# Performance work log

Measured on AMD Instinct MI355X. Metric: run time of the kernel, lower is better.

Reference implementation:

```python
import jax, jax.numpy as jnp
import numpy as np

# dims
N, T = 16, 2000            # batch, encoder frames
ENC, DEC = 512, 512        # enc_dim, dec_dim
ATT, C, K, H = 512, 10, 64, 4  # att_dim, conv_channels, loc_context, att_head


def setup_inputs() -> dict:
    key = jax.random.key(0)
    ks = jax.random.split(key, 16)
    s = 0.02
    enc_pad = jax.random.normal(ks[0], (N, T, ENC), jnp.float32)
    enc_len = jax.random.randint(ks[1], (N,), T // 2, T + 1, jnp.int32)
    dec_prev = jax.random.normal(ks[2], (N, DEC), jnp.float32)
    ali_prev = jax.random.uniform(ks[3], (N, H, T), jnp.float32)
    ali_prev = ali_prev / ali_prev.sum(-1, keepdims=True)
    # parameters (torch layout)
    We = jax.random.normal(ks[4], (ATT * H, ENC), jnp.float32) * s   # enc_proj weight
    be = jnp.zeros((ATT * H,), jnp.float32)                          # enc_proj bias
    Wk = jax.random.normal(ks[5], (ATT * H, ENC), jnp.float32) * s   # key_proj
    Wd = jax.random.normal(ks[6], (ATT * H, DEC), jnp.float32) * s   # dec_proj
    WF = jax.random.normal(ks[7], (C * H, 1, 2 * K + 1), jnp.float32) * s  # F: grouped conv1d
    bF = jnp.zeros((C * H,), jnp.float32)
    Wa = jax.random.normal(ks[8], (H, ATT, C), jnp.float32) * s      # att: 1x1 grouped conv, per-head [ATT,C]
    Ww = jax.random.normal(ks[9], (H, ATT), jnp.float32) * s         # w: 1x1 grouped conv, per-head [ATT]
    Wc = jax.random.normal(ks[10], (ENC, ATT * H), jnp.float32) * s  # ctx_proj
    bc = jnp.zeros((ENC,), jnp.float32)
    return {"enc_pad": enc_pad, "enc_len": enc_len, "dec_prev": dec_prev,
            "ali_prev": ali_prev, "We": We, "be": be, "Wk": Wk, "Wd": Wd,
            "WF": WF, "bF": bF, "Wa": Wa, "Ww": Ww, "Wc": Wc, "bc": bc}


def reference(enc_pad, enc_len, dec_prev, ali_prev, We, be, Wk, Wd, WF, bF, Wa, Ww, Wc, bc):
    n, t, _ = enc_pad.shape
    # enc_part: N x H x T x D
    ep = enc_pad @ We.T + be
    enc_part = ep.reshape(n, t, H, ATT).transpose(0, 2, 1, 3)
    # key_part: N x H x D x T (matches torch transpose(1,2).view ordering)
    kp = enc_pad @ Wk.T
    key_part = kp.transpose(0, 2, 1).reshape(n, H, ATT, t)
    # pad mask: N x T, True where padded
    pad_mask = jnp.arange(t)[None, :] >= enc_len[:, None]
    # location features: grouped conv1d over alignment, per head
    f = jax.lax.conv_general_dilated(
        ali_prev, WF, window_strides=(1,), padding=[(K, K)],
        dimension_numbers=("NCH", "OIH", "NCH"), feature_group_count=H)
    f = (f + bF[None, :, None]).reshape(n, H, C, t)
    # 1x1 grouped conv: C -> ATT per head
    att_part = jnp.einsum("hdc,nhct->nhdt", Wa, f)
    dec_part = (dec_prev @ Wd.T).reshape(n, H, ATT)
    sum_part = jnp.tanh(att_part + key_part + dec_part[..., None])  # N x H x D x T
    score = jnp.einsum("hd,nhdt->nht", Ww, sum_part)                # N x H x T
    score = jnp.where(pad_mask[:, None, :], -jnp.inf, score)
    ali = jax.nn.softmax(score, axis=-1)
    ctx = jnp.einsum("nht,nhtd->nhd", ali, enc_part).reshape(n, H * ATT)
    ctx = ctx @ Wc.T + bc
    return ali, ctx
```

## Files before the change

### kernel.cpp

```cpp
#include <hip/hip_runtime.h>

#define NB   16
#define TT   2000
#define TP   2048
#define SPT  2048
#define ENC  512
#define ATTD 512
#define HH   4
#define CC   10
#define KK   64
#define KW   129
#define HATT 2048

typedef unsigned short u16;
typedef __attribute__((ext_vector_type(8))) short bf16x8;
typedef __attribute__((ext_vector_type(4))) float f32x4;

#define AS1 __attribute__((address_space(1)))
#define AS3 __attribute__((address_space(3)))

__device__ inline unsigned bfpack2(float lo, float hi) {
    unsigned a = __builtin_bit_cast(unsigned, lo);
    unsigned b = __builtin_bit_cast(unsigned, hi);
    a = (a + 0x7fffu + ((a >> 16) & 1u)) >> 16;
    b = (b + 0x7fffu + ((b >> 16) & 1u)) >> 16;
    return a | (b << 16);
}

__global__ __launch_bounds__(256) void prep_kernel(
    const float* __restrict__ enc, const float* __restrict__ Wk,
    const float* __restrict__ ali_prev, const float* __restrict__ WF,
    const float* __restrict__ bF, const float* __restrict__ dec_prev,
    const float* __restrict__ Wd, const float* __restrict__ Wa,
    const int* __restrict__ enc_len,
    u16* __restrict__ Abf, u16* __restrict__ Wkbf,
    u16* __restrict__ ftb, u16* __restrict__ wab,
    float* __restrict__ decp)
{
    __shared__ union {
        struct { float aliW[632]; float wfT[KW * CC]; float bfs[CC]; } cv;
        float dsl[16 * 128];
    } sm;
    const int bid = blockIdx.x, tid = threadIdx.x;

    if (bid < 8704) {
        long long gid = ((long long)bid * 256 + tid) * 8;
        const long long ATOT = (long long)NB * TP * ENC;
        if (gid < ATOT) {
            int n = (int)(gid >> 20);
            int rem = (int)(gid & ((1 << 20) - 1));
            int r = rem >> 9, e = rem & 511;
            if (r < enc_len[n]) {
                const float* s = enc + ((long long)n * TT + r) * ENC + e;
                float4 v0 = *(const float4*)s;
                float4 v1 = *(const float4*)(s + 4);
                uint4 out;
                out.x = bfpack2(v0.x, v0.y); out.y = bfpack2(v0.z, v0.w);
                out.z = bfpack2(v1.x, v1.y); out.w = bfpack2(v1.z, v1.w);
                *(uint4*)(Abf + gid) = out;
            }
        } else {
            long long j = gid - ATOT;
            const float* s = Wk + j;
            float4 v0 = *(const float4*)s;
            float4 v1 = *(const float4*)(s + 4);
            uint4 out;
            out.x = bfpack2(v0.x, v0.y); out.y = bfpack2(v0.z, v0.w);
            out.z = bfpack2(v1.x, v1.y); out.w = bfpack2(v1.z, v1.w);
            *(uint4*)(Wkbf + j) = out;
        }
    } else if (bid < 8960) {
        int b2 = bid - 8704;
        int tc = b2 & 3, h = (b2 >> 2) & 3, n = b2 >> 4;
        int t0 = tc * 500;
        float* aliW = sm.cv.aliW;
        float* wfT  = sm.cv.wfT;
        float* bfs  = sm.cv.bfs;
        const float* arow = ali_prev + ((long long)n * HH + h) * TT;
        for (int i = tid; i < 632; i += 256) {
            int tt = t0 - KK + i;
            aliW[i] = (tt >= 0 && tt < TT) ? arow[tt] : 0.f;
        }
        for (int i = tid; i < KW * CC; i += 256) {
            int k = i / CC, c = i - k * CC;
            wfT[i] = WF[(h * CC + c) * KW + k];
        }
        if (tid < CC) bfs[tid] = bF[h * CC + tid];
        __syncthreads();
        if (tid < 250) {
            float acc0[CC], acc1[CC];
            #pragma unroll
            for (int c = 0; c < CC; c++) { acc0[c] = 0.f; acc1[c] = 0.f; }
            const int base = 2 * tid;
            float2 w0 = *(const float2*)&aliW[base];
            for (int k = 0; k < 128; k += 2) {
                float2 w2 = *(const float2*)&aliW[base + k + 2];
                #pragma unroll
                for (int cj = 0; cj < 5; cj++) {
                    float2 fk  = *(const float2*)&wfT[k * CC + cj * 2];
                    float2 fk1 = *(const float2*)&wfT[(k + 1) * CC + cj * 2];
                    acc0[2*cj]   += w0.x * fk.x + w0.y * fk1.x;
                    acc0[2*cj+1] += w0.x * fk.y + w0.y * fk1.y;
                    acc1[2*cj]   += w0.y * fk.x + w2.x * fk1.x;
                    acc1[2*cj+1] += w0.y * fk.y + w2.x * fk1.y;
                }
                w0 = w2;
            }
            #pragma unroll
            for (int cj = 0; cj < 5; cj++) {
                float2 fk = *(const float2*)&wfT[128 * CC + cj * 2];
                acc0[2*cj]   += w0.x * fk.x;  acc0[2*cj+1] += w0.x * fk.y;
                acc1[2*cj]   += w0.y * fk.x;  acc1[2*cj+1] += w0.y * fk.y;
            }
            #pragma unroll
            for (int c = 0; c < CC; c++) { acc0[c] += bfs[c]; acc1[c] += bfs[c]; }
            int t = t0 + base;
            u16* frow = ftb + (((long long)(n * HH + h)) * TP + t) * 16;
            uint4 ra, rb;
            ra.x = bfpack2(acc0[0], acc0[1]); ra.y = bfpack2(acc0[2], acc0[3]);
            ra.z = bfpack2(acc0[4], acc0[5]); ra.w = bfpack2(acc0[6], acc0[7]);
            rb.x = bfpack2(acc0[8], acc0[9]); rb.y = 0u; rb.z = 0u; rb.w = 0u;
            *(uint4*)(frow)     = ra; *(uint4*)(frow + 8)  = rb;
            ra.x = bfpack2(acc1[0], acc1[1]); ra.y = bfpack2(acc1[2], acc1[3]);
            ra.z = bfpack2(acc1[4], acc1[5]); ra.w = bfpack2(acc1[6], acc1[7]);
            rb.x = bfpack2(acc1[8], acc1[9]);
            *(uint4*)(frow + 16) = ra; *(uint4*)(frow + 24) = rb;
        } else if (tc == 3) {
            uint4 z = {0u, 0u, 0u, 0u};
            int r0 = 2000 + (tid - 250) * 8;
            u16* frow = ftb + (((long long)(n * HH + h)) * TP + r0) * 16;
            for (int r = 0; r < 8; r++) {
                *(uint4*)(frow + r * 16)     = z;
                *(uint4*)(frow + r * 16 + 8) = z;
            }
        }
    } else if (bid < 8992) {
        int b2 = bid - 8960;
        int kc = b2 >> 3, jc = b2 & 7;
        for (int i = tid; i < 2048; i += 256) {
            int nn = i >> 7, kk = i & 127;
            sm.dsl[i] = dec_prev[nn * 512 + kc * 128 + kk];
        }
        __syncthreads();
        int d = jc * 256 + tid;
        float acc[NB];
        #pragma unroll
        for (int n = 0; n < NB; n++) acc[n] = 0.f;
        const float4* w4 = (const float4*)(Wd + (long long)d * 512 + kc * 128);
        for (int e4 = 0; e4 < 32; e4++) {
            float4 w = w4[e4];
            #pragma unroll
            for (int n = 0; n < NB; n++) {
                const float* a = sm.dsl + n * 128 + e4 * 4;
                acc[n] += w.x * a[0] + w.y * a[1] + w.z * a[2] + w.w * a[3];
            }
        }
        #pragma unroll
        for (int n = 0; n < NB; n++) decp[((long long)kc * NB + n) * HATT + d] = acc[n];
    } else {
        int b2 = bid - 8992;
        int j0 = b2 * 512 + tid * 2;
        #pragma unroll
        for (int q = 0; q < 2; q++) {
            int j = j0 + q;
            int hh = j >> 9, dd = j & 511;
            const float* wr = Wa + ((long long)(hh * ATTD + dd)) * CC;
            uint4 ra, rb;
            ra.x = bfpack2(wr[0], wr[1]); ra.y = bfpack2(wr[2], wr[3]);
            ra.z = bfpack2(wr[4], wr[5]); ra.w = bfpack2(wr[6], wr[7]);
            rb.x = bfpack2(wr[8], wr[9]); rb.y = 0u; rb.z = 0u; rb.w = 0u;
            u16* out = wab + (long long)j * 16;
            *(uint4*)(out)     = ra;
            *(uint4*)(out + 8) = rb;
        }
    }
}

__global__ __launch_bounds__(256, 4) void score_gemm_kernel(
    const u16* __restrict__ Abf, const u16* __restrict__ Bbf,
    const u16* __restrict__ ftb, const u16* __restrict__ wab,
    const float* __restrict__ decp, const float* __restrict__ Ww,
    const int* __restrict__ enc_len, float* __restrict__ score_part)
{
    __shared__ __attribute__((aligned(16))) char smem[40960];
    float* sred = (float*)smem;

    const int bid = blockIdx.x;
    const int xcd = bid & 7;
    const int lcl = bid >> 3;
    const int nt = lcl & 15;
    const int rr = lcl >> 4;
    const int n = rr >> 1, half = rr & 1;
    const int mtl = (xcd + n) & 7;
    const int mt = half ? (8 + mtl) : mtl;

    if (mt * 128 >= enc_len[n]) return;

    const int tid = threadIdx.x, wave = tid >> 6, lane = tid & 63;
    const int l16 = lane & 15, lk = lane >> 4;
    const int h = nt >> 2;

    const u16* Aptr = Abf + ((long long)n * TP + mt * 128) * ENC;
    const u16* Bptr = Bbf + (long long)nt * 128 * ENC;

    f32x4 acc[4][4];
    #pragma unroll
    for (int mi = 0; mi < 4; mi++)
        #pragma unroll
        for (int nj = 0; nj < 4; nj++) {
            f32x4 z = {0.f, 0.f, 0.f, 0.f};
            acc[mi][nj] = z;
        }

    const int wrow = (wave >> 1) * 64, wcol = (wave & 1) * 64;
    const int t0 = mt * 128, dd0 = (nt & 3) * 128;

    {
        const char* eAsrc = (const char*)(ftb + (((long long)(n * HH + h)) * TP + t0) * 16);
        const char* eBsrc = (const char*)(wab + (long long)nt * 128 * 16);
        __builtin_amdgcn_global_load_lds(
            (const AS1 void*)(eAsrc + tid * 16),
            (AS3 void*)(smem + 32768 + wave * 1024), 16, 0, 0);
        __builtin_amdgcn_global_load_lds(
            (const AS1 void*)(eBsrc + tid * 16),
            (AS3 void*)(smem + 36864 + wave * 1024), 16, 0, 0);
    }

    for (int kt = 0; kt < 8; kt++) {
        const int k0 = kt * 64;
        #pragma unroll
        for (int i = 0; i < 4; i++) {
            int b = i * 4096 + tid * 16;
            int r = b >> 7, kb = b & 127;
            int kbs = kb ^ ((r & 7) << 4);
            __builtin_amdgcn_global_load_lds(
                (const AS1 void*)(Aptr + r * ENC + k0 + (kbs >> 1)),
                (AS3 void*)(smem + i * 4096 + wave * 1024), 16, 0, 0);
            __builtin_amdgcn_global_load_lds(
                (const AS1 void*)(Bptr + r * ENC + k0 + (kbs >> 1)),
                (AS3 void*)(smem + 16384 + i * 4096 + wave * 1024), 16, 0, 0);
        }
        __syncthreads();
        #pragma unroll
        for (int ks = 0; ks < 64; ks += 32) {
            bf16x8 af[4], bf[4];
            #pragma unroll
            for (int mi = 0; mi < 4; mi++) {
                int row = wrow + mi * 16 + l16;
                int cb = (ks * 2 + lk * 16) ^ ((row & 7) << 4);
                af[mi] = *(const bf16x8*)(smem + row * 128 + cb);
            }
            #pragma unroll
            for (int nj = 0; nj < 4; nj++) {
                int row = wcol + nj * 16 + l16;
                int cb = (ks * 2 + lk * 16) ^ ((row & 7) << 4);
                bf[nj] = *(const bf16x8*)(smem + 16384 + row * 128 + cb);
            }
            #pragma unroll
            for (int mi = 0; mi < 4; mi++)
                #pragma unroll
                for (int nj = 0; nj < 4; nj++)
                    acc[mi][nj] = __builtin_amdgcn_mfma_f32_16x16x32_bf16(
                        af[mi], bf[nj], acc[mi][nj], 0, 0, 0);
        }
        __syncthreads();
    }

    {
        const u16* eA = (const u16*)(smem + 32768);
        const u16* eB = (const u16*)(smem + 36864);
        bf16x8 zer = {0, 0, 0, 0, 0, 0, 0, 0};
        bf16x8 af[4], bf[4];
        #pragma unroll
        for (int mi = 0; mi < 4; mi++) {
            af[mi] = zer;
            if (lk < 2) af[mi] = *(const bf16x8*)(eA + (wrow + mi * 16 + l16) * 16 + lk * 8);
        }
        #pragma unroll
        for (int nj = 0; nj < 4; nj++) {
            bf[nj] = zer;
            if (lk < 2) bf[nj] = *(const bf16x8*)(eB + (wcol + nj * 16 + l16) * 16 + lk * 8);
        }
        #pragma unroll
        for (int mi = 0; mi < 4; mi++)
            #pragma unroll
            for (int nj = 0; nj < 4; nj++)
                acc[mi][nj] = __builtin_amdgcn_mfma_f32_16x16x32_bf16(
                    af[mi], bf[nj], acc[mi][nj], 0, 0, 0);
    }

    float wm2[4], dec4[4];
    #pragma unroll
    for (int nj = 0; nj < 4; nj++) {
        int cl = wcol + nj * 16 + l16;
        wm2[nj] = -2.f * Ww[h * ATTD + dd0 + cl];
        int j = nt * 128 + cl;
        dec4[nj] = decp[((long long)0 * NB + n) * HATT + j]
                 + decp[((long long)1 * NB + n) * HATT + j]
                 + decp[((long long)2 * NB + n) * HATT + j]
                 + decp[((long long)3 * NB + n) * HATT + j];
    }

    #pragma unroll
    for (int mi = 0; mi < 4; mi++) {
        #pragma unroll
        for (int j = 0; j < 4; j++) {
            int rl = wrow + mi * 16 + lk * 4 + j;
            float s = 0.f;
            #pragma unroll
            for (int nj = 0; nj < 4; nj++) {
                float v = acc[mi][nj][j] + dec4[nj];
                float e = __expf(v + v);
                s = fmaf(wm2[nj], __builtin_amdgcn_rcpf(e + 1.f), s);
            }
            s += __shfl_xor(s, 1); s += __shfl_xor(s, 2);
            s += __shfl_xor(s, 4); s += __shfl_xor(s, 8);
            if (l16 == 0) sred[(wave & 1) * 128 + rl] = s;
        }
    }
    __syncthreads();
    if (tid < 128) {
        int t = t0 + tid;
        if (t < TT)
            score_part[((long long)((nt & 3) * NB + n) * HH + h) * SPT + t] =
                sred[tid] + sred[128 + tid];
    }
}

__global__ __launch_bounds__(256) void softmax_kernel(
    const float* __restrict__ score_part, const int* __restrict__ enc_len,
    float* __restrict__ ali)
{
    int n = blockIdx.x >> 2, h = blockIdx.x & 3;
    int len = enc_len[n];
    int tid = threadIdx.x;
    int t0 = tid * 8;
    float s[8];
    #pragma unroll
    for (int i = 0; i < 8; i++) s[i] = 0.f;
    #pragma unroll
    for (int q = 0; q < 4; q++) {
        const float* rb = score_part + (((long long)(q * NB + n)) * HH + h) * SPT + t0;
        float4 a = *(const float4*)rb;
        float4 b = *(const float4*)(rb + 4);
        s[0] += a.x; s[1] += a.y; s[2] += a.z; s[3] += a.w;
        s[4] += b.x; s[5] += b.y; s[6] += b.z; s[7] += b.w;
    }
    float lmax = -3.4e38f;
    #pragma unroll
    for (int i = 0; i < 8; i++) {
        if (t0 + i < len) lmax = fmaxf(lmax, s[i]);
    }
    __shared__ float red[256];
    red[tid] = lmax; __syncthreads();
    for (int off = 128; off; off >>= 1) {
        if (tid < off) red[tid] = fmaxf(red[tid], red[tid + off]);
        __syncthreads();
    }
    float bmax = red[0];
    __syncthreads();
    float lsum = 0.f;
    #pragma unroll
    for (int i = 0; i < 8; i++) {
        if (t0 + i < len) { s[i] = expf(s[i] - bmax); lsum += s[i]; }
        else s[i] = 0.f;
    }
    red[tid] = lsum; __syncthreads();
    for (int off = 128; off; off >>= 1) {
        if (tid < off) red[tid] += red[tid + off];
        __syncthreads();
    }
    float inv = 1.f / red[0];
    float* arow = ali + ((long long)n * HH + h) * TT;
    if (t0 + 8 <= TT) {
        float4 o0 = {s[0] * inv, s[1] * inv, s[2] * inv, s[3] * inv};
        float4 o1 = {s[4] * inv, s[5] * inv, s[6] * inv, s[7] * inv};
        *(float4*)(arow + t0) = o0;
        *(float4*)(arow + t0 + 4) = o1;
    } else {
        for (int i = 0; i < 8; i++)
            if (t0 + i < TT) arow[t0 + i] = s[i] * inv;
    }
}

__global__ __launch_bounds__(256) void a_enc_kernel(
    const float* __restrict__ ali, const u16* __restrict__ Abf,
    const int* __restrict__ enc_len, float* __restrict__ aep)
{
    int tc = blockIdx.x & 31, n = blockIdx.x >> 5;
    int tid = threadIdx.x;
    int len = enc_len[n];
    int tbeg = tc * 63;
    int cnt = len - tbeg; if (cnt > 63) cnt = 63; if (cnt < 0) cnt = 0;
    __shared__ float aliS[HH][64];
    __shared__ float red[2][4][129];
    {
        int hh = tid >> 6, tt = tid & 63;
        aliS[hh][tt] = (tt < cnt) ? ali[((long long)n * HH + hh) * TT + tbeg + tt] : 0.f;
    }
    __syncthreads();
    const int l = tid & 127, tq = tid >> 7;
    float acc[HH][4];
    #pragma unroll
    for (int hh = 0; hh < HH; hh++)
        #pragma unroll
        for (int k = 0; k < 4; k++) acc[hh][k] = 0.f;
    for (int ii = 0; ii < 32; ii++) {
        int tl = ii * 2 + tq;
        if (tl < cnt) {
            uint2 u = *(const uint2*)(Abf + ((long long)n * TP + tbeg + tl) * ENC + l * 4);
            float e0 = __builtin_bit_cast(float, u.x << 16);
            float e1 = __builtin_bit_cast(float, u.x & 0xffff0000u);
            float e2 = __builtin_bit_cast(float, u.y << 16);
            float e3 = __builtin_bit_cast(float, u.y & 0xffff0000u);
            #pragma unroll
            for (int hh = 0; hh < HH; hh++) {
                float w = aliS[hh][tl];
                acc[hh][0] += w * e0; acc[hh][1] += w * e1;
                acc[hh][2] += w * e2; acc[hh][3] += w * e3;
            }
        }
    }
    #pragma unroll
    for (int hh = 0; hh < HH; hh++) {
        __syncthreads();
        #pragma unroll
        for (int k = 0; k < 4; k++) red[tq][k][l] = acc[hh][k];
        __syncthreads();
        int d2 = tid * 2;
        float v0 = red[0][d2 & 3][d2 >> 2] + red[1][d2 & 3][d2 >> 2];
        int d3 = d2 + 1;
        float v1 = red[0][d3 & 3][d3 >> 2] + red[1][d3 & 3][d3 >> 2];
        float2 o = {v0, v1};
        *(float2*)(aep + (((long long)tc * NB + n) * HH + hh) * ENC + d2) = o;
    }
}

__global__ __launch_bounds__(256) void ctx_tmp_kernel(
    const float* __restrict__ aep, const float* __restrict__ We,
    const float* __restrict__ be, float* __restrict__ ctmp)
{
    int kc = blockIdx.x >> 3, jc = blockIdx.x & 7;
    int tid = threadIdx.x;
    int j = jc * 256 + tid;
    int h = j >> 9;
    __shared__ float aes[16 * 64];
    for (int i = tid; i < 1024; i += 256) {
        int nn = i >> 6, kk = i & 63;
        float s = 0.f;
        for (int tc = 0; tc < 32; tc++)
            s += aep[(((long long)tc * NB + nn) * HH + h) * ENC + kc * 64 + kk];
        aes[i] = s;
    }
    __syncthreads();
    float acc[NB];
    #pragma unroll
    for (int n = 0; n < NB; n++) acc[n] = 0.f;
    const float4* w4 = (const float4*)(We + (long long)j * 512 + kc * 64);
    for (int e4 = 0; e4 < 16; e4++) {
        float4 w = w4[e4];
        #pragma unroll
        for (int n = 0; n < NB; n++) {
            const float* a = aes + n * 64 + e4 * 4;
            acc[n] += w.x * a[0] + w.y * a[1] + w.z * a[2] + w.w * a[3];
        }
    }
    float bias = (kc == 0) ? be[j] : 0.f;
    #pragma unroll
    for (int n = 0; n < NB; n++)
        ctmp[((long long)kc * NB + n) * HATT + j] = acc[n] + bias;
}

__global__ __launch_bounds__(256) void ctx_out_kernel(
    const float* __restrict__ ctmp, const float* __restrict__ Wc,
    const float* __restrict__ bc, float* __restrict__ out_ctx)
{
    int ec = blockIdx.x & 15, nc = blockIdx.x >> 4;
    int tid = threadIdx.x;
    __shared__ float ct[8 * 2048];
    __shared__ float red[8][8][33];
    for (int i = tid; i < 8 * 2048; i += 256) {
        int nn = i >> 11, j = i & 2047;
        int n = nc * 8 + nn;
        float s = 0.f;
        #pragma unroll
        for (int kc = 0; kc < 8; kc++)
            s += ctmp[((long long)kc * NB + n) * HATT + j];
        ct[i] = s;
    }
    __syncthreads();
    int eo = tid & 31, kq = tid >> 5;
    int eg = ec * 32 + eo;
    float acc[8];
    #pragma unroll
    for (int nn = 0; nn < 8; nn++) acc[nn] = 0.f;
    const float4* w4 = (const float4*)(Wc + (long long)eg * HATT + kq * 256);
    for (int j4 = 0; j4 < 64; j4++) {
        float4 w = w4[j4];
        #pragma unroll
        for (int nn = 0; nn < 8; nn++) {
            const float* a = ct + nn * 2048 + kq * 256 + j4 * 4;
            acc[nn] += w.x * a[0] + w.y * a[1] + w.z * a[2] + w.w * a[3];
        }
    }
    #pragma unroll
    for (int nn = 0; nn < 8; nn++) red[kq][nn][eo] = acc[nn];
    __syncthreads();
    {
        int eo2 = tid & 31, nn2 = tid >> 5;
        float s = 0.f;
        #pragma unroll
        for (int kq2 = 0; kq2 < 8; kq2++) s += red[kq2][nn2][eo2];
        out_ctx[((long long)(nc * 8 + nn2)) * 512 + ec * 32 + eo2] = s + bc[ec * 32 + eo2];
    }
}

extern "C" void kernel_launch(void* const* d_in, const int* in_sizes, int n_in,
                              void* d_out, int out_size, void* d_ws, size_t ws_size,
                              hipStream_t stream)
{
    (void)in_sizes; (void)n_in; (void)out_size; (void)ws_size;
    const float* enc_pad  = (const float*)d_in[0];
    const int*   enc_len  = (const int*)  d_in[1];
    const float* dec_prev = (const float*)d_in[2];
    const float* ali_prev = (const float*)d_in[3];
    const float* We = (const float*)d_in[4];
    const float* be = (const float*)d_in[5];
    const float* Wk = (const float*)d_in[6];
    const float* Wd = (const float*)d_in[7];
    const float* WF = (const float*)d_in[8];
    const float* bF = (const float*)d_in[9];
    const float* Wa = (const float*)d_in[10];
    const float* Ww = (const float*)d_in[11];
    const float* Wc = (const float*)d_in[12];
    const float* bc = (const float*)d_in[13];

    char* ws = (char*)d_ws;
    u16*   Abf  = (u16*)  (ws);
    u16*   Wkbf = (u16*)  (ws + 33554432);
    u16*   ftb  = (u16*)  (ws + 35651584);
    u16*   wab  = (u16*)  (ws + 39845888);
    float* decp = (float*)(ws + 39911424);
    float* spart= (float*)(ws + 40435712);
    float* aep  = (float*)(ws + 40435712);
    float* ctmp = (float*)(ws + 35651584);

    float* ali = (float*)d_out;
    float* ctx = (float*)d_out + NB * HH * TT;

    prep_kernel      <<<8996, 256, 0, stream>>>(enc_pad, Wk, ali_prev, WF, bF,
                                                dec_prev, Wd, Wa, enc_len,
                                                Abf, Wkbf, ftb, wab, decp);
    score_gemm_kernel<<<4096, 256, 0, stream>>>(Abf, Wkbf, ftb, wab, decp, Ww,
                                                enc_len, spart);
    softmax_kernel   <<<64,   256, 0, stream>>>(spart, enc_len, ali);
    a_enc_kernel     <<<512,  256, 0, stream>>>(ali, Abf, enc_len, aep);
    ctx_tmp_kernel   <<<64,   256, 0, stream>>>(aep, We, be, ctmp);
    ctx_out_kernel   <<<32,   256, 0, stream>>>(ctmp, Wc, bc, ctx);
}
```

Baseline: 174.4 us.

## Cut GEMM LDS footprint, raise occupancy, split launch, use nontemporal loads

The score GEMM no longer stages the extra location-feature operand tiles in shared memory; they are read straight from global memory into registers, which shrinks LDS from 40 KB to 32 KB. Launch bounds go from 4 to 5 blocks per CU so more blocks can be resident. The GEMM grid is also split into two launches of 2048 blocks each, and the prep kernel's fp32 reads of enc_pad and Wk become nontemporal loads. In exchange, the direct global loads add latency at the end of the K loop, the tighter launch bound may cause register spills, and the second launch adds its own launch cost.

After: 274.4 us. 57.3% more time.

```diff
diff --git a/kernel.cpp b/kernel.cpp
--- a/kernel.cpp
+++ b/kernel.cpp
@@ -51,9 +51,9 @@
             int rem = (int)(gid & ((1 << 20) - 1));
             int r = rem >> 9, e = rem & 511;
             if (r < enc_len[n]) {
-                const float* s = enc + ((long long)n * TT + r) * ENC + e;
-                float4 v0 = *(const float4*)s;
-                float4 v1 = *(const float4*)(s + 4);
+                const f32x4* s = (const f32x4*)(enc + ((long long)n * TT + r) * ENC + e);
+                f32x4 v0 = __builtin_nontemporal_load(s);
+                f32x4 v1 = __builtin_nontemporal_load(s + 1);
                 uint4 out;
                 out.x = bfpack2(v0.x, v0.y); out.y = bfpack2(v0.z, v0.w);
                 out.z = bfpack2(v1.x, v1.y); out.w = bfpack2(v1.z, v1.w);
@@ -61,9 +61,9 @@
             }
         } else {
             long long j = gid - ATOT;
-            const float* s = Wk + j;
-            float4 v0 = *(const float4*)s;
-            float4 v1 = *(const float4*)(s + 4);
+            const f32x4* s = (const f32x4*)(Wk + j);
+            f32x4 v0 = __builtin_nontemporal_load(s);
+            f32x4 v1 = __builtin_nontemporal_load(s + 1);
             uint4 out;
             out.x = bfpack2(v0.x, v0.y); out.y = bfpack2(v0.z, v0.w);
             out.z = bfpack2(v1.x, v1.y); out.w = bfpack2(v1.z, v1.w);
@@ -176,16 +176,17 @@
     }
 }
 
-__global__ __launch_bounds__(256, 4) void score_gemm_kernel(
+__global__ __launch_bounds__(256, 5) void score_gemm_kernel(
     const u16* __restrict__ Abf, const u16* __restrict__ Bbf,
     const u16* __restrict__ ftb, const u16* __restrict__ wab,
     const float* __restrict__ decp, const float* __restrict__ Ww,
-    const int* __restrict__ enc_len, float* __restrict__ score_part)
-{
-    __shared__ __attribute__((aligned(16))) char smem[40960];
+    const int* __restrict__ enc_len, float* __restrict__ score_part,
+    int bidBase)
+{
+    __shared__ __attribute__((aligned(16))) char smem[32768];
     float* sred = (float*)smem;
 
-    const int bid = blockIdx.x;
+    const int bid = blockIdx.x + bidBase;
     const int xcd = bid & 7;
     const int lcl = bid >> 3;
     const int nt = lcl & 15;
@@ -214,17 +215,6 @@
 
     const int wrow = (wave >> 1) * 64, wcol = (wave & 1) * 64;
     const int t0 = mt * 128, dd0 = (nt & 3) * 128;
-
-    {
-        const char* eAsrc = (const char*)(ftb + (((long long)(n * HH + h)) * TP + t0) * 16);
-        const char* eBsrc = (const char*)(wab + (long long)nt * 128 * 16);
-        __builtin_amdgcn_global_load_lds(
-            (const AS1 void*)(eAsrc + tid * 16),
-            (AS3 void*)(smem + 32768 + wave * 1024), 16, 0, 0);
-        __builtin_amdgcn_global_load_lds(
-            (const AS1 void*)(eBsrc + tid * 16),
-            (AS3 void*)(smem + 36864 + wave * 1024), 16, 0, 0);
-    }
 
     for (int kt = 0; kt < 8; kt++) {
         const int k0 = kt * 64;
@@ -267,19 +257,21 @@
     }
 
     {
-        const u16* eA = (const u16*)(smem + 32768);
-        const u16* eB = (const u16*)(smem + 36864);
         bf16x8 zer = {0, 0, 0, 0, 0, 0, 0, 0};
         bf16x8 af[4], bf[4];
         #pragma unroll
-        for (int mi = 0; mi < 4; mi++) {
-            af[mi] = zer;
-            if (lk < 2) af[mi] = *(const bf16x8*)(eA + (wrow + mi * 16 + l16) * 16 + lk * 8);
-        }
-        #pragma unroll
-        for (int nj = 0; nj < 4; nj++) {
-            bf[nj] = zer;
-            if (lk < 2) bf[nj] = *(const bf16x8*)(eB + (wcol + nj * 16 + l16) * 16 + lk * 8);
+        for (int mi = 0; mi < 4; mi++) af[mi] = zer;
+        #pragma unroll
+        for (int nj = 0; nj < 4; nj++) bf[nj] = zer;
+        if (lk < 2) {
+            #pragma unroll
+            for (int mi = 0; mi < 4; mi++)
+                af[mi] = *(const bf16x8*)(ftb +
+                    (((long long)(n * HH + h)) * TP + t0 + wrow + mi * 16 + l16) * 16 + lk * 8);
+            #pragma unroll
+            for (int nj = 0; nj < 4; nj++)
+                bf[nj] = *(const bf16x8*)(wab +
+                    ((long long)(nt * 128 + wcol + nj * 16 + l16)) * 16 + lk * 8);
         }
         #pragma unroll
         for (int mi = 0; mi < 4; mi++)
@@ -551,8 +543,10 @@
     prep_kernel      <<<8996, 256, 0, stream>>>(enc_pad, Wk, ali_prev, WF, bF,
                                                 dec_prev, Wd, Wa, enc_len,
                                                 Abf, Wkbf, ftb, wab, decp);
-    score_gemm_kernel<<<4096, 256, 0, stream>>>(Abf, Wkbf, ftb, wab, decp, Ww,
-                                                enc_len, spart);
+    score_gemm_kernel<<<2048, 256, 0, stream>>>(Abf, Wkbf, ftb, wab, decp, Ww,
+                                                enc_len, spart, 0);
+    score_gemm_kernel<<<2048, 256, 0, stream>>>(Abf, Wkbf, ftb, wab, decp, Ww,
+                                                enc_len, spart, 2048);
     softmax_kernel   <<<64,   256, 0, stream>>>(spart, enc_len, ali);
     a_enc_kernel     <<<512,  256, 0, stream>>>(ali, Abf, enc_len, aep);
     ctx_tmp_kernel   <<<64,   256, 0, stream>>>(aep, We, be, ctmp);
```
